# Kernel tuning notes

Measured on AMD Instinct MI355X. Metric: run time of the kernel, lower is better.

The kernel has to match this reference:

```python
import jax, jax.numpy as jnp
import numpy as np

LN_EPS = 1e-5
EPS = 1e-8
NUM_ITERS = 3

def _ln(x, w, b):
    mu = jnp.mean(x, axis=-1, keepdims=True)
    var = jnp.var(x, axis=-1, keepdims=True)
    return (x - mu) * jax.lax.rsqrt(var + LN_EPS) * w + b

def setup_inputs() -> dict:
    key = jax.random.key(0)
    ks = jax.random.split(key, 20)
    B, H, W, C = 16, 64, 64, 256
    D, S, HID, T = 128, 10, 256, 20
    g = lambda k, *shape: jax.random.normal(k, shape, dtype=jnp.float32) * 0.02
    return {
        'obs': jax.random.normal(ks[0], (B, H, W, C), dtype=jnp.float32),
        'noise': jax.random.normal(ks[1], (B, S, D), dtype=jnp.float32),
        'slots_mu': jax.random.normal(ks[2], (1, 1, D), dtype=jnp.float32),
        'slots_log_sigma': jax.random.normal(ks[3], (1, 1, D), dtype=jnp.float32) * 0.1,
        'ni_w': jnp.ones((C,), jnp.float32), 'ni_b': jnp.zeros((C,), jnp.float32),
        'ns_w': jnp.ones((D,), jnp.float32), 'ns_b': jnp.zeros((D,), jnp.float32),
        'nm_w': jnp.ones((D,), jnp.float32), 'nm_b': jnp.zeros((D,), jnp.float32),
        'Wq': g(ks[4], D, D), 'Wk': g(ks[5], C, D), 'Wv': g(ks[6], C, D),
        'mlp_w1': g(ks[7], D, 2 * D), 'mlp_b1': jnp.zeros((2 * D,), jnp.float32),
        'mlp_w2': g(ks[8], 2 * D, D), 'mlp_b2': jnp.zeros((D,), jnp.float32),
        'pd_w1': g(ks[9], D, HID), 'pd_b1': jnp.zeros((HID,), jnp.float32),
        'pd_w2': g(ks[10], HID, D), 'pd_b2': jnp.zeros((D,), jnp.float32),
        'tc_w': g(ks[11], D, T), 'tc_b': jnp.zeros((T,), jnp.float32),
    }

def reference(obs, noise, slots_mu, slots_log_sigma, ni_w, ni_b, ns_w, ns_b,
              nm_w, nm_b, Wq, Wk, Wv, mlp_w1, mlp_b1, mlp_w2, mlp_b2,
              pd_w1, pd_b1, pd_w2, pd_b2, tc_w, tc_b):
    B = obs.shape[0]
    x = obs.reshape(B, -1, obs.shape[-1])  # [B, N, C] (flatten H,W)
    D = Wq.shape[0]
    # slot init: mu + sigma * noise
    slots = slots_mu + jnp.exp(slots_log_sigma) * noise  # [B, S, D]
    x = _ln(x, ni_w, ni_b)
    k = x @ Wk  # [B, N, D]
    v = x @ Wv  # [B, N, D]
    scale = D ** -0.5
    attn = None
    for _ in range(NUM_ITERS):
        slots_prev = slots
        q = _ln(slots, ns_w, ns_b) @ Wq  # [B, S, D]
        logits = jnp.einsum('bsd,bnd->bsn', q, k) * scale
        attn = jax.nn.softmax(logits, axis=1)  # competitive over slots
        w = attn / (jnp.sum(attn, axis=-1, keepdims=True) + EPS)
        updates = jnp.einsum('bsn,bnd->bsd', w, v)
        slots = slots_prev + updates
        h = _ln(slots, nm_w, nm_b)
        slots = slots + (jax.nn.relu(h @ mlp_w1 + mlp_b1) @ mlp_w2 + mlp_b2)
    objects = jax.nn.relu(slots @ pd_w1 + pd_b1) @ pd_w2 + pd_b2
    object_types = slots @ tc_w + tc_b
    return objects, object_types
```

## Files before the change

kernel.cpp:

```cpp
#include <hip/hip_runtime.h>
#include <hip/hip_bf16.h>

typedef __hip_bfloat16 bf16;
typedef __attribute__((ext_vector_type(8))) short bf16x8;
typedef __attribute__((ext_vector_type(4))) float f32x4;

#define LN_EPS 1e-5f
#define ATT_EPS 1e-8f

__device__ __forceinline__ float bflo(unsigned u){ union{unsigned i;float f;}c; c.i=u<<16; return c.f; }
__device__ __forceinline__ float bfhi(unsigned u){ union{unsigned i;float f;}c; c.i=u&0xffff0000u; return c.f; }
__device__ __forceinline__ float bf2f(bf16 h){ return __bfloat162float(h); }
__device__ __forceinline__ unsigned f2bfbits(float f){
    bf16 h = __float2bfloat16(f);
    unsigned short s; __builtin_memcpy(&s, &h, 2);
    return (unsigned)s;
}

__device__ __forceinline__ float getv(const void* p, long i, int isf){
    if (isf) return ((const float*)p)[i];
    return bf2f(((const bf16*)p)[i]);
}
__device__ __forceinline__ void get8(const void* p, long i, int isf, float* o){
    if (isf){
        __builtin_memcpy(o, (const float*)p + i, 32);
    } else {
        unsigned u[4];
        __builtin_memcpy(u, (const bf16*)p + i, 16);
        o[0]=bflo(u[0]); o[1]=bfhi(u[0]); o[2]=bflo(u[1]); o[3]=bfhi(u[1]);
        o[4]=bflo(u[2]); o[5]=bfhi(u[2]); o[6]=bflo(u[3]); o[7]=bfhi(u[3]);
    }
}
__device__ __forceinline__ void load4f(const float* p, float* o){ __builtin_memcpy(o, p, 16); }
__device__ __forceinline__ void store4f(float* p, const float* v){ __builtin_memcpy(p, v, 16); }

__device__ __forceinline__ void wred2(float& a, float& b){
    #pragma unroll
    for (int m = 32; m > 0; m >>= 1){
        a += __shfl_xor(a, m, 64);
        b += __shfl_xor(b, m, 64);
    }
}

__global__ __launch_bounds__(256) void k_gmat(
        const void* __restrict__ Wq, const void* __restrict__ Wk,
        const void* __restrict__ niw, int* __restrict__ flag,
        float* __restrict__ G){
    unsigned u0; __builtin_memcpy(&u0, niw, 4);
    int isf = (u0 == 0x3F800000u) ? 1 : 0;
    if (blockIdx.x == 0 && threadIdx.x == 0) *flag = isf;
    int c = blockIdx.x, t = threadIdx.x;
    int d = t & 127, half = t >> 7;
    __shared__ float red2[2][128];
    float acc = 0.f;
    #pragma unroll
    for (int ch = 0; ch < 8; ch++){
        int dp = half*64 + ch*8;
        float wq8[8], wk8[8];
        get8(Wq, (long)d*128 + dp, isf, wq8);
        get8(Wk, (long)c*128 + dp, isf, wk8);
        #pragma unroll
        for (int j=0;j<8;j++) acc += wq8[j]*wk8[j];
    }
    red2[half][d] = acc;
    __syncthreads();
    if (t < 128)
        G[(long)t*256 + c] = (red2[0][t] + red2[1][t]) * 0.08838834764831845f;
}

__device__ __forceinline__ void phaseD(
        int b, int s, int t, const float* shlns, const float* __restrict__ G,
        const void* __restrict__ niw, const void* __restrict__ nib, int isf,
        bf16* __restrict__ wkqb, float* __restrict__ Ug, float* __restrict__ Vg,
        float* __restrict__ P2, float* __restrict__ t0g, float* __restrict__ t1g,
        float* redUV){
    int c = t;
    float kqc = 0.f;
    for (int d0 = 0; d0 < 128; d0 += 8){
        float l8[8];
        load4f(shlns + d0, l8); load4f(shlns + d0 + 4, l8 + 4);
        kqc += l8[0]*G[(long)(d0+0)*256+c] + l8[1]*G[(long)(d0+1)*256+c]
             + l8[2]*G[(long)(d0+2)*256+c] + l8[3]*G[(long)(d0+3)*256+c]
             + l8[4]*G[(long)(d0+4)*256+c] + l8[5]*G[(long)(d0+5)*256+c]
             + l8[6]*G[(long)(d0+6)*256+c] + l8[7]*G[(long)(d0+7)*256+c];
    }
    float wc = getv(niw, c, isf), bc = getv(nib, c, isf);
    float wkq = wc*kqc, vq = bc*kqc;
    float uu = wkq, vv = vq;
    wred2(uu, vv);
    int wid = t >> 6, lane = t & 63;
    if (lane == 0){ redUV[wid*2] = uu; redUV[wid*2+1] = vv; }
    wkqb[((long)b*16 + s)*256 + c] = __float2bfloat16(wkq);
    int bs = b*10 + s;
    P2[bs*256 + c] = 0.f;
    __syncthreads();
    if (t == 0){
        Ug[bs] = redUV[0] + redUV[2] + redUV[4] + redUV[6];
        Vg[bs] = redUV[1] + redUV[3] + redUV[5] + redUV[7];
        t0g[bs] = 0.f; t1g[bs] = 0.f;
    }
}

__global__ __launch_bounds__(256) void k_prep(
        const void* __restrict__ noise, const void* __restrict__ smu,
        const void* __restrict__ sls, const void* __restrict__ nsw,
        const void* __restrict__ nsb, const void* __restrict__ niw,
        const void* __restrict__ nib, const int* __restrict__ flag,
        const float* __restrict__ G, float* __restrict__ slots,
        bf16* __restrict__ wkqb, float* __restrict__ Ug, float* __restrict__ Vg,
        float* __restrict__ P2, float* __restrict__ t0g, float* __restrict__ t1g){
    int isf = *flag;
    int bs = blockIdx.x, t = threadIdx.x;
    int b = bs/10, s = bs - b*10;
    __shared__ __align__(16) float shlns[128];
    __shared__ float red[2][2];
    __shared__ float redUV[8];
    if (t < 128){
        float sv = getv(smu,t,isf) + __expf(getv(sls,t,isf)) * getv(noise,(long)bs*128+t,isf);
        slots[bs*128 + t] = sv;
        shlns[t] = sv;
        float su = sv, sq = sv*sv;
        wred2(su, sq);
        int wid = t >> 6, lane = t & 63;
        if (lane == 0){ red[wid][0]=su; red[wid][1]=sq; }
    }
    __syncthreads();
    if (t < 128){
        float su = red[0][0]+red[1][0], sq = red[0][1]+red[1][1];
        float m = su*(1.f/128.f), var = sq*(1.f/128.f) - m*m;
        float ri = rsqrtf(var + LN_EPS);
        shlns[t] = (shlns[t] - m)*ri*getv(nsw,t,isf) + getv(nsb,t,isf);
    }
    __syncthreads();
    phaseD(b, s, t, shlns, G, niw, nib, isf, wkqb, Ug, Vg, P2, t0g, t1g, redUV);
    if (s == 0){
        #pragma unroll
        for (int r = 10; r < 16; r++)
            wkqb[((long)b*16 + r)*256 + t] = __float2bfloat16(0.f);
    }
}

__global__ __launch_bounds__(256) void k_attn5(
        const void* __restrict__ obs, const bf16* __restrict__ wkqb,
        const float* __restrict__ Ug, const float* __restrict__ Vg,
        const int* __restrict__ flag, float* __restrict__ P2,
        float* __restrict__ t0g, float* __restrict__ t1g){
    int isf = *flag;
    int tile = blockIdx.x, b = blockIdx.y, t = threadIdx.x;
    int w = t >> 6, l = t & 63;
    __shared__ unsigned sxn[64*132];
    __shared__ __align__(16) float attnP[64*12];
    __shared__ float muri[128];
    __shared__ float denp0[4][16], denp1[4][16];

    if (isf){
        const float* gx = (const float*)obs + ((long)b*4096 + tile*64)*256;
        #pragma unroll
        for (int i = 0; i < 8; i++){
            int Ld = t*4 + i*1024;
            int px = Ld >> 7, col = Ld & 127;
            float f8[8];
            __builtin_memcpy(f8, gx + (long)px*256 + col*2, 32);
            unsigned pk[4];
            #pragma unroll
            for (int k2=0;k2<4;k2++)
                pk[k2] = (f2bfbits(f8[2*k2+1])<<16) | f2bfbits(f8[2*k2]);
            __builtin_memcpy(&sxn[px*132 + col], pk, 16);
        }
    } else {
        const unsigned* gx = (const unsigned*)obs + ((long)b*4096 + tile*64)*128;
        #pragma unroll
        for (int i = 0; i < 8; i++){
            int Ld = t*4 + i*1024;
            int px = Ld >> 7, col = Ld & 127;
            unsigned tmp[4];
            __builtin_memcpy(tmp, gx + Ld, 16);
            __builtin_memcpy(&sxn[px*132 + col], tmp, 16);
        }
    }
    bf16x8 bfr[8];
    {
        int s = l & 15, q = (l >> 4) & 3;
        const bf16* base = wkqb + ((long)b*16 + s)*256 + q*8;
        #pragma unroll
        for (int ks = 0; ks < 8; ks++)
            __builtin_memcpy(&bfr[ks], base + ks*32, 16);
    }
    __syncthreads();

    {
        int px = t >> 2, q = t & 3;
        float su = 0.f, sq = 0.f;
        #pragma unroll
        for (int j = 0; j < 8; j++){
            unsigned d4[4];
            __builtin_memcpy(d4, &sxn[px*132 + q*32 + j*4], 16);
            #pragma unroll
            for (int k2=0;k2<4;k2++){
                float a0 = bflo(d4[k2]), a1 = bfhi(d4[k2]);
                su += a0 + a1; sq += a0*a0 + a1*a1;
            }
        }
        su += __shfl_xor(su,1,64); sq += __shfl_xor(sq,1,64);
        su += __shfl_xor(su,2,64); sq += __shfl_xor(sq,2,64);
        if (q == 0){
            float m = su*(1.f/256.f);
            float ri = rsqrtf(sq*(1.f/256.f) - m*m + LN_EPS);
            muri[px*2] = m; muri[px*2+1] = ri;
        }
    }
    __syncthreads();

    f32x4 acc = {0.f,0.f,0.f,0.f};
    {
        int m = l & 15, q = (l >> 4) & 3;
        int rowbase = (w*16 + m)*132;
        #pragma unroll
        for (int ks = 0; ks < 8; ks++){
            bf16x8 af;
            __builtin_memcpy(&af, &sxn[rowbase + ks*16 + q*4], 16);
            acc = __builtin_amdgcn_mfma_f32_16x16x32_bf16(af, bfr[ks], acc, 0, 0, 0);
        }
    }

    {
        int col = l & 15, q = (l >> 4) & 3;
        float Uv = 0.f, Vv = 0.f;
        if (col < 10){ Uv = Ug[b*10 + col]; Vv = Vg[b*10 + col]; }
        float pden0 = 0.f, pden1 = 0.f;
        #pragma unroll
        for (int reg = 0; reg < 4; reg++){
            int px = w*16 + q*4 + reg;
            float mr[2]; __builtin_memcpy(mr, &muri[px*2], 8);
            float lg = (col < 10) ? (mr[1]*acc[reg] - mr[1]*mr[0]*Uv + Vv) : -1e30f;
            float mx = lg;
            mx = fmaxf(mx, __shfl_xor(mx,1,64));
            mx = fmaxf(mx, __shfl_xor(mx,2,64));
            mx = fmaxf(mx, __shfl_xor(mx,4,64));
            mx = fmaxf(mx, __shfl_xor(mx,8,64));
            float e = (col < 10) ? __expf(lg - mx) : 0.f;
            float sm = e;
            sm += __shfl_xor(sm,1,64);
            sm += __shfl_xor(sm,2,64);
            sm += __shfl_xor(sm,4,64);
            sm += __shfl_xor(sm,8,64);
            float a = e / sm;
            if (col < 10) attnP[px*12 + col] = a*mr[1];
            pden0 += a;
            pden1 += a*mr[1]*mr[0];
        }
        pden0 += __shfl_xor(pden0,16,64); pden0 += __shfl_xor(pden0,32,64);
        pden1 += __shfl_xor(pden1,16,64); pden1 += __shfl_xor(pden1,32,64);
        if (l < 10){ denp0[w][l] = pden0; denp1[w][l] = pden1; }
    }
    __syncthreads();
    if (t < 10){
        atomicAdd(&t0g[b*10 + t], denp0[0][t]+denp0[1][t]+denp0[2][t]+denp0[3][t]);
        atomicAdd(&t1g[b*10 + t], denp1[0][t]+denp1[1][t]+denp1[2][t]+denp1[3][t]);
    }

    {
        int c = t, ch = c >> 1, hh = c & 1;
        float pacc[10];
        #pragma unroll
        for (int s=0;s<10;s++) pacc[s]=0.f;
        for (int n = 0; n < 64; n++){
            unsigned d = sxn[n*132 + ch];
            float xv = hh ? bfhi(d) : bflo(d);
            float a[10];
            load4f(&attnP[n*12], a);
            load4f(&attnP[n*12 + 4], a + 4);
            __builtin_memcpy(a + 8, &attnP[n*12 + 8], 8);
            #pragma unroll
            for (int s=0;s<10;s++) pacc[s] += a[s]*xv;
        }
        #pragma unroll
        for (int s=0;s<10;s++) atomicAdd(&P2[b*2560 + s*256 + c], pacc[s]);
    }
}

__global__ __launch_bounds__(256) void k_slot(
        float* __restrict__ slots, float* __restrict__ P2,
        float* __restrict__ t0g, float* __restrict__ t1g,
        const void* __restrict__ Wv,
        const void* __restrict__ nmw, const void* __restrict__ nmb,
        const void* __restrict__ w1, const void* __restrict__ b1,
        const void* __restrict__ w2, const void* __restrict__ b2,
        const void* __restrict__ nsw, const void* __restrict__ nsb,
        const void* __restrict__ niw, const void* __restrict__ nib,
        const void* __restrict__ pw1, const void* __restrict__ pb1,
        const void* __restrict__ pw2, const void* __restrict__ pb2,
        const void* __restrict__ tw, const void* __restrict__ tb,
        const int* __restrict__ flag, const float* __restrict__ G,
        bf16* __restrict__ wkqb, float* __restrict__ Ug, float* __restrict__ Vg,
        void* __restrict__ out, int last){
    int isf = *flag;
    int bs = blockIdx.x, t = threadIdx.x;
    int b = bs/10, s = bs - b*10;
    __shared__ __align__(16) float pr[256];
    __shared__ __align__(16) float redA[16*128];
    __shared__ __align__(16) float redB[8*256];
    __shared__ __align__(16) float redT[8*32];
    __shared__ __align__(16) float hld[128];
    __shared__ __align__(16) float hid[256];
    __shared__ __align__(16) float shlns[128];
    __shared__ float red[4][2];
    __shared__ float redUV[8];

    float t0v = t0g[bs], t1v = t1g[bs];
    float wc = getv(niw,t,isf), bcv = getv(nib,t,isf);
    pr[t] = (P2[bs*256 + t] - t1v)*wc + t0v*bcv;
    __syncthreads();

    {
        int g = t & 15, ks = t >> 4;
        int d0 = g*8;
        float a8[8] = {0,0,0,0,0,0,0,0};
        #pragma unroll
        for (int j=0;j<16;j++){
            int c2 = ks*16 + j;
            float w8[8]; get8(Wv, (long)c2*128 + d0, isf, w8);
            float pv = pr[c2];
            #pragma unroll
            for (int k=0;k<8;k++) a8[k] += pv*w8[k];
        }
        store4f(&redA[ks*128 + d0], a8);
        store4f(&redA[ks*128 + d0 + 4], a8+4);
    }
    __syncthreads();
    float dv = t0v + ATT_EPS;
    float sn = 0.f;
    if (t < 128){
        float u = 0.f;
        #pragma unroll
        for (int ks=0;ks<16;ks++) u += redA[ks*128 + t];
        sn = slots[bs*128 + t] + u/dv;
    }
    float v = (t < 128) ? sn : 0.f;
    float su = v, sq = v*v;
    wred2(su, sq);
    int wid = t >> 6, lane = t & 63;
    if (lane == 0){ red[wid][0]=su; red[wid][1]=sq; }
    __syncthreads();
    su = red[0][0]+red[1][0]+red[2][0]+red[3][0];
    sq = red[0][1]+red[1][1]+red[2][1]+red[3][1];
    float mu = su*(1.f/128.f), var = sq*(1.f/128.f) - mu*mu;
    float rinv = rsqrtf(var + LN_EPS);
    if (t < 128) hld[t] = (v-mu)*rinv*getv(nmw,t,isf) + getv(nmb,t,isf);
    __syncthreads();

    {
        int g = t & 31, ks = t >> 5;
        int h0 = g*8;
        float a8[8] = {0,0,0,0,0,0,0,0};
        #pragma unroll
        for (int j=0;j<16;j++){
            int d = ks*16 + j;
            float w8[8]; get8(w1, (long)d*256 + h0, isf, w8);
            float hv = hld[d];
            #pragma unroll
            for (int k=0;k<8;k++) a8[k] += hv*w8[k];
        }
        store4f(&redB[ks*256 + h0], a8);
        store4f(&redB[ks*256 + h0 + 4], a8+4);
    }
    __syncthreads();
    {
        float hb = getv(b1,t,isf);
        #pragma unroll
        for (int ks=0;ks<8;ks++) hb += redB[ks*256 + t];
        hid[t] = fmaxf(hb, 0.f);
    }
    __syncthreads();

    {
        int g = t & 15, ks = t >> 4;
        int d0 = g*8;
        float a8[8] = {0,0,0,0,0,0,0,0};
        #pragma unroll
        for (int j=0;j<16;j++){
            int h = ks*16 + j;
            float w8[8]; get8(w2, (long)h*128 + d0, isf, w8);
            float hv = hid[h];
            #pragma unroll
            for (int k=0;k<8;k++) a8[k] += hv*w8[k];
        }
        store4f(&redA[ks*128 + d0], a8);
        store4f(&redA[ks*128 + d0 + 4], a8+4);
    }
    __syncthreads();
    float v2 = 0.f;
    if (t < 128){
        float o = getv(b2,t,isf);
        #pragma unroll
        for (int ks=0;ks<16;ks++) o += redA[ks*128 + t];
        v2 = sn + o;
    }

    if (!last){
        if (t < 128) slots[bs*128 + t] = v2;
        float s2 = v2, ss2 = v2*v2;
        wred2(s2, ss2);
        if (lane == 0){ red[wid][0]=s2; red[wid][1]=ss2; }
        __syncthreads();
        s2 = red[0][0]+red[1][0]+red[2][0]+red[3][0];
        ss2 = red[0][1]+red[1][1]+red[2][1]+red[3][1];
        float mu2 = s2*(1.f/128.f), var2 = ss2*(1.f/128.f) - mu2*mu2;
        float ri2 = rsqrtf(var2 + LN_EPS);
        if (t < 128)
            shlns[t] = (v2 - mu2)*ri2*getv(nsw,t,isf) + getv(nsb,t,isf);
        __syncthreads();
        phaseD(b, s, t, shlns, G, niw, nib, isf, wkqb, Ug, Vg, P2, t0g, t1g, redUV);
    } else {
        if (t < 128) shlns[t] = v2;
        __syncthreads();
        {
            int g = t & 31, ks = t >> 5;
            int h0 = g*8;
            float a8[8] = {0,0,0,0,0,0,0,0};
            #pragma unroll
            for (int j=0;j<16;j++){
                int d = ks*16 + j;
                float w8[8]; get8(pw1, (long)d*256 + h0, isf, w8);
                float hv = shlns[d];
                #pragma unroll
                for (int k=0;k<8;k++) a8[k] += hv*w8[k];
            }
            store4f(&redB[ks*256 + h0], a8);
            store4f(&redB[ks*256 + h0 + 4], a8+4);
        }
        __syncthreads();
        {
            float hb = getv(pb1,t,isf);
            #pragma unroll
            for (int ks=0;ks<8;ks++) hb += redB[ks*256 + t];
            hid[t] = fmaxf(hb, 0.f);
        }
        __syncthreads();
        {
            int g = t & 15, ks = t >> 4;
            int d0 = g*8;
            float a8[8] = {0,0,0,0,0,0,0,0};
            #pragma unroll
            for (int j=0;j<16;j++){
                int h = ks*16 + j;
                float w8[8]; get8(pw2, (long)h*128 + d0, isf, w8);
                float hv = hid[h];
                #pragma unroll
                for (int k=0;k<8;k++) a8[k] += hv*w8[k];
            }
            store4f(&redA[ks*128 + d0], a8);
            store4f(&redA[ks*128 + d0 + 4], a8+4);
        }
        {
            int ot = t & 31, ks = t >> 5;
            float a = 0.f;
            if (ot < 20){
                #pragma unroll
                for (int j=0;j<16;j++){
                    int d = ks*16 + j;
                    a += shlns[d]*getv(tw, (long)d*20 + ot, isf);
                }
            }
            redT[ks*32 + ot] = a;
        }
        __syncthreads();
        if (t < 128){
            float o = getv(pb2,t,isf);
            #pragma unroll
            for (int ks=0;ks<16;ks++) o += redA[ks*128 + t];
            int idx = bs*128 + t;
            if (isf) ((float*)out)[idx] = o; else ((bf16*)out)[idx] = __float2bfloat16(o);
        }
        if (t < 20){
            float o = getv(tb,t,isf);
            #pragma unroll
            for (int ks=0;ks<8;ks++) o += redT[ks*32 + t];
            int idx = 16*10*128 + bs*20 + t;
            if (isf) ((float*)out)[idx] = o; else ((bf16*)out)[idx] = __float2bfloat16(o);
        }
    }
}

extern "C" void kernel_launch(void* const* d_in, const int* in_sizes, int n_in,
                              void* d_out, int out_size, void* d_ws, size_t ws_size,
                              hipStream_t stream) {
    const void* obs   = d_in[0];
    const void* noise = d_in[1];
    const void* smu   = d_in[2];
    const void* sls   = d_in[3];
    const void* niw   = d_in[4];
    const void* nib   = d_in[5];
    const void* nsw   = d_in[6];
    const void* nsb   = d_in[7];
    const void* nmw   = d_in[8];
    const void* nmb   = d_in[9];
    const void* Wq    = d_in[10];
    const void* Wk    = d_in[11];
    const void* Wv    = d_in[12];
    const void* w1    = d_in[13];
    const void* b1    = d_in[14];
    const void* w2    = d_in[15];
    const void* b2    = d_in[16];
    const void* pw1   = d_in[17];
    const void* pb1   = d_in[18];
    const void* pw2   = d_in[19];
    const void* pb2   = d_in[20];
    const void* tw    = d_in[21];
    const void* tb    = d_in[22];

    char* ws = (char*)d_ws;
    int*   flag  = (int*)(ws);
    float* t0g   = (float*)(ws + 1024);
    float* t1g   = (float*)(ws + 2048);
    float* Ug    = (float*)(ws + 3072);
    float* Vg    = (float*)(ws + 4096);
    float* slots = (float*)(ws + 5120);
    float* P2    = (float*)(ws + 87040);
    float* G     = (float*)(ws + 250880);
    bf16*  wkqb  = (bf16*) (ws + 381952);

    k_gmat<<<256, 256, 0, stream>>>(Wq, Wk, niw, flag, G);
    k_prep<<<160, 256, 0, stream>>>(noise, smu, sls, nsw, nsb, niw, nib, flag, G,
                                    slots, wkqb, Ug, Vg, P2, t0g, t1g);
    for (int it = 0; it < 3; it++){
        k_attn5<<<dim3(64, 16), 256, 0, stream>>>(obs, wkqb, Ug, Vg, flag, P2, t0g, t1g);
        k_slot<<<160, 256, 0, stream>>>(slots, P2, t0g, t1g, Wv, nmw, nmb,
                                        w1, b1, w2, b2, nsw, nsb, niw, nib,
                                        pw1, pb1, pw2, pb2, tw, tb, flag, G,
                                        wkqb, Ug, Vg, d_out, (it == 2) ? 1 : 0);
    }
}
```

Before: 238.8 us.

## Precompute bf16 K/V projections once and stream compact KV in attention iterations

Adds a path that projects the layer-normed observations to bf16 K and V once, using a split hi/lo bf16 MFMA of the LN-folded weights. The three attention iterations then read this 256-wide bf16 KV buffer instead of re-reading the full obs tensor with the folded Wk·Wq form. Queries are computed per slot and stored as bf16, and per-tile partial updates are reduced in the slot kernel. The path is chosen only when the workspace is at least 41 MB, which costs an extra large buffer and some bf16 rounding of K, V and q.

```diff
diff --git a/kernel.cpp b/kernel.cpp
--- a/kernel.cpp
+++ b/kernel.cpp
@@ -41,6 +41,7 @@
         b += __shfl_xor(b, m, 64);
     }
 }
+
 
 __global__ __launch_bounds__(256) void k_gmat(
         const void* __restrict__ Wq, const void* __restrict__ Wk,
@@ -482,6 +483,454 @@
     }
 }
 
+
+__global__ __launch_bounds__(256) void k_wprep(
+        const void* __restrict__ Wk, const void* __restrict__ Wv,
+        const void* __restrict__ niw, const void* __restrict__ nib,
+        int* __restrict__ flag, bf16* __restrict__ Whit, bf16* __restrict__ Wlot,
+        float* __restrict__ Sg, float* __restrict__ Bg){
+    int d = blockIdx.x, t = threadIdx.x;
+    unsigned u0; __builtin_memcpy(&u0, niw, 4);
+    int isf = (u0 == 0x3F800000u) ? 1 : 0;
+    if (d == 0 && t == 0) *flag = isf;
+    float val = (d < 128) ? getv(Wk, (long)t*128 + d, isf)
+                          : getv(Wv, (long)t*128 + (d-128), isf);
+    float wp = getv(niw, t, isf) * val;
+    bf16 h = __float2bfloat16(wp);
+    Whit[(long)d*256 + t] = h;
+    Wlot[(long)d*256 + t] = __float2bfloat16(wp - bf2f(h));
+    float s = wp, bb = getv(nib, t, isf) * val;
+    wred2(s, bb);
+    __shared__ float r2[8];
+    int wv = t >> 6, ln = t & 63;
+    if (ln == 0){ r2[wv*2] = s; r2[wv*2+1] = bb; }
+    __syncthreads();
+    if (t == 0){ Sg[d] = r2[0]+r2[2]+r2[4]+r2[6]; Bg[d] = r2[1]+r2[3]+r2[5]+r2[7]; }
+}
+
+__global__ __launch_bounds__(256) void k_pre(
+        const void* __restrict__ obs, const int* __restrict__ flag,
+        const bf16* __restrict__ Whit, const bf16* __restrict__ Wlot,
+        const float* __restrict__ Sg, const float* __restrict__ Bg,
+        bf16* __restrict__ kvg){
+    int isf = *flag;
+    int tile = blockIdx.x, t = threadIdx.x;
+    __shared__ unsigned sxn[64*132];
+    __shared__ float muri[128];
+    __shared__ __align__(16) float sS[256];
+    __shared__ __align__(16) float sB[256];
+
+    if (isf){
+        const float* gx = (const float*)obs + (long)tile*64*256;
+        #pragma unroll
+        for (int i = 0; i < 8; i++){
+            int Ld = t*4 + i*1024;
+            int px = Ld >> 7, col = Ld & 127;
+            float f8[8];
+            __builtin_memcpy(f8, gx + (long)px*256 + col*2, 32);
+            unsigned pk[4];
+            #pragma unroll
+            for (int k2=0;k2<4;k2++)
+                pk[k2] = (f2bfbits(f8[2*k2+1])<<16) | f2bfbits(f8[2*k2]);
+            __builtin_memcpy(&sxn[px*132 + col], pk, 16);
+        }
+    } else {
+        const unsigned* gx = (const unsigned*)obs + (long)tile*64*128;
+        #pragma unroll
+        for (int i = 0; i < 8; i++){
+            int Ld = t*4 + i*1024;
+            int px = Ld >> 7, col = Ld & 127;
+            unsigned tmp[4];
+            __builtin_memcpy(tmp, gx + Ld, 16);
+            __builtin_memcpy(&sxn[px*132 + col], tmp, 16);
+        }
+    }
+    sS[t] = Sg[t]; sB[t] = Bg[t];
+    __syncthreads();
+    {
+        int px = t >> 2, q = t & 3;
+        float su = 0.f, sq = 0.f;
+        #pragma unroll
+        for (int j = 0; j < 8; j++){
+            unsigned d4[4];
+            __builtin_memcpy(d4, &sxn[px*132 + q*32 + j*4], 16);
+            #pragma unroll
+            for (int k2=0;k2<4;k2++){
+                float a0 = bflo(d4[k2]), a1 = bfhi(d4[k2]);
+                su += a0 + a1; sq += a0*a0 + a1*a1;
+            }
+        }
+        su += __shfl_xor(su,1,64); sq += __shfl_xor(sq,1,64);
+        su += __shfl_xor(su,2,64); sq += __shfl_xor(sq,2,64);
+        if (q == 0){
+            float m = su*(1.f/256.f);
+            float ri = rsqrtf(sq*(1.f/256.f) - m*m + LN_EPS);
+            muri[px*2] = m; muri[px*2+1] = ri;
+        }
+    }
+    __syncthreads();
+    {
+        int l = t & 63, w = t >> 6;
+        int mcol = l & 15, q4 = l >> 4;
+        unsigned* kvo = (unsigned*)kvg;
+        #pragma unroll
+        for (int mt = 0; mt < 4; mt++){
+            int dl = w*64 + mt*16 + mcol;
+            const bf16* ah = Whit + (long)dl*256 + q4*8;
+            const bf16* al = Wlot + (long)dl*256 + q4*8;
+            bf16x8 afh[8], afl[8];
+            #pragma unroll
+            for (int ks = 0; ks < 8; ks++){
+                __builtin_memcpy(&afh[ks], ah + ks*32, 16);
+                __builtin_memcpy(&afl[ks], al + ks*32, 16);
+            }
+            #pragma unroll
+            for (int ct = 0; ct < 4; ct++){
+                f32x4 a = {0.f,0.f,0.f,0.f};
+                int rb = (ct*16 + mcol)*132;
+                #pragma unroll
+                for (int ks = 0; ks < 8; ks++){
+                    bf16x8 bx;
+                    __builtin_memcpy(&bx, &sxn[rb + ks*16 + q4*4], 16);
+                    a = __builtin_amdgcn_mfma_f32_16x16x32_bf16(afh[ks], bx, a, 0,0,0);
+                    a = __builtin_amdgcn_mfma_f32_16x16x32_bf16(afl[ks], bx, a, 0,0,0);
+                }
+                int px = ct*16 + mcol;
+                int d0 = w*64 + mt*16 + q4*4;
+                float mu = muri[px*2], ri = muri[px*2+1];
+                float o0 = ri*a[0] - ri*mu*sS[d0+0] + sB[d0+0];
+                float o1 = ri*a[1] - ri*mu*sS[d0+1] + sB[d0+1];
+                float o2 = ri*a[2] - ri*mu*sS[d0+2] + sB[d0+2];
+                float o3 = ri*a[3] - ri*mu*sS[d0+3] + sB[d0+3];
+                long base = (long)tile*8192 + (long)px*128 + (d0>>1);
+                kvo[base]   = (f2bfbits(o1)<<16) | f2bfbits(o0);
+                kvo[base+1] = (f2bfbits(o3)<<16) | f2bfbits(o2);
+            }
+        }
+    }
+}
+
+__global__ __launch_bounds__(256) void k_prep2(
+        const void* __restrict__ noise, const void* __restrict__ smu,
+        const void* __restrict__ sls, const void* __restrict__ nsw,
+        const void* __restrict__ nsb, const void* __restrict__ Wq,
+        const int* __restrict__ flag, float* __restrict__ slots,
+        bf16* __restrict__ qb, float* __restrict__ t0g){
+    int isf = *flag;
+    int bs = blockIdx.x, t = threadIdx.x;
+    int b = bs/10, s = bs - b*10;
+    __shared__ __align__(16) float shlns[128];
+    __shared__ float red[2][2];
+    if (t < 128){
+        float sv = getv(smu,t,isf) + __expf(getv(sls,t,isf)) * getv(noise,(long)bs*128+t,isf);
+        slots[bs*128 + t] = sv;
+        shlns[t] = sv;
+        float su = sv, sq = sv*sv;
+        wred2(su, sq);
+        int wid = t >> 6, lane = t & 63;
+        if (lane == 0){ red[wid][0]=su; red[wid][1]=sq; }
+    }
+    __syncthreads();
+    if (t < 128){
+        float su = red[0][0]+red[1][0], sq = red[0][1]+red[1][1];
+        float m = su*(1.f/128.f), var = sq*(1.f/128.f) - m*m;
+        float ri = rsqrtf(var + LN_EPS);
+        shlns[t] = (shlns[t] - m)*ri*getv(nsw,t,isf) + getv(nsb,t,isf);
+    }
+    __syncthreads();
+    if (t < 128){
+        float acc = 0.f;
+        #pragma unroll 8
+        for (int dp = 0; dp < 128; dp++)
+            acc += shlns[dp] * getv(Wq, (long)dp*128 + t, isf);
+        qb[((long)b*16 + s)*128 + t] = __float2bfloat16(acc * 0.08838834764831845f);
+    }
+    if (t == 0) t0g[bs] = 0.f;
+    if (s == 0 && t < 128){
+        #pragma unroll
+        for (int r = 10; r < 16; r++)
+            qb[((long)b*16 + r)*128 + t] = __float2bfloat16(0.f);
+    }
+}
+
+__global__ __launch_bounds__(256) void k_attn6(
+        const bf16* __restrict__ kvg, const bf16* __restrict__ qb,
+        float* __restrict__ t0g, float* __restrict__ P2p){
+    int tile = blockIdx.x, b = blockIdx.y, t = threadIdx.x;
+    int w = t >> 6, l = t & 63;
+    __shared__ unsigned sxn[64*132];
+    __shared__ __align__(16) float attnP[64*16];
+    __shared__ float denp0[4][16];
+
+    const unsigned* gx = (const unsigned*)(kvg + ((long)b*4096 + tile*64)*256);
+    #pragma unroll
+    for (int i = 0; i < 8; i++){
+        int Ld = t*4 + i*1024;
+        int px = Ld >> 7, col = Ld & 127;
+        unsigned tmp[4];
+        __builtin_memcpy(tmp, gx + Ld, 16);
+        __builtin_memcpy(&sxn[px*132 + col], tmp, 16);
+    }
+    bf16x8 bfr[4];
+    {
+        int s = l & 15, q = (l >> 4) & 3;
+        const bf16* base = qb + ((long)b*16 + s)*128 + q*8;
+        #pragma unroll
+        for (int ks = 0; ks < 4; ks++)
+            __builtin_memcpy(&bfr[ks], base + ks*32, 16);
+    }
+    __syncthreads();
+
+    f32x4 acc = {0.f,0.f,0.f,0.f};
+    {
+        int m = l & 15, q = (l >> 4) & 3;
+        int rowbase = (w*16 + m)*132;
+        #pragma unroll
+        for (int ks = 0; ks < 4; ks++){
+            bf16x8 af;
+            __builtin_memcpy(&af, &sxn[rowbase + ks*16 + q*4], 16);
+            acc = __builtin_amdgcn_mfma_f32_16x16x32_bf16(af, bfr[ks], acc, 0, 0, 0);
+        }
+    }
+    {
+        int col = l & 15;
+        int q = (l >> 4) & 3;
+        float pden0 = 0.f;
+        #pragma unroll
+        for (int reg = 0; reg < 4; reg++){
+            int px = w*16 + q*4 + reg;
+            float lg = (col < 10) ? acc[reg] : -1e30f;
+            float mx = lg;
+            mx = fmaxf(mx, __shfl_xor(mx,1,64));
+            mx = fmaxf(mx, __shfl_xor(mx,2,64));
+            mx = fmaxf(mx, __shfl_xor(mx,4,64));
+            mx = fmaxf(mx, __shfl_xor(mx,8,64));
+            float e = (col < 10) ? __expf(lg - mx) : 0.f;
+            float sm = e;
+            sm += __shfl_xor(sm,1,64);
+            sm += __shfl_xor(sm,2,64);
+            sm += __shfl_xor(sm,4,64);
+            sm += __shfl_xor(sm,8,64);
+            float a = e / sm;
+            if (col < 10) attnP[px*16 + (col < 5 ? col : col + 3)] = a;
+            pden0 += a;
+        }
+        pden0 += __shfl_xor(pden0,16,64); pden0 += __shfl_xor(pden0,32,64);
+        if (l < 10) denp0[w][l] = pden0;
+    }
+    __syncthreads();
+    if (t < 10)
+        atomicAdd(&t0g[b*10 + t], denp0[0][t]+denp0[1][t]+denp0[2][t]+denp0[3][t]);
+
+    {
+        int d = t & 127, grp = t >> 7;
+        float p0=0.f,p1=0.f,p2=0.f,p3=0.f,p4=0.f;
+        int vdw = 64 + (d >> 1);
+        int hh = d & 1;
+        #pragma unroll 4
+        for (int n = 0; n < 64; n++){
+            unsigned dw = sxn[n*132 + vdw];
+            float xv = hh ? bfhi(dw) : bflo(dw);
+            float a4[4];
+            load4f(&attnP[n*16 + grp*8], a4);
+            float a5 = attnP[n*16 + grp*8 + 4];
+            p0 += a4[0]*xv; p1 += a4[1]*xv; p2 += a4[2]*xv; p3 += a4[3]*xv; p4 += a5*xv;
+        }
+        long base = ((long)(b*10 + grp*5)*64 + tile)*128 + d;
+        P2p[base]            = p0;
+        P2p[base +   64*128] = p1;
+        P2p[base + 2*64*128] = p2;
+        P2p[base + 3*64*128] = p3;
+        P2p[base + 4*64*128] = p4;
+    }
+}
+
+__global__ __launch_bounds__(256) void k_slot2(
+        float* __restrict__ slots, const float* __restrict__ P2p,
+        float* __restrict__ t0g,
+        const void* __restrict__ nmw, const void* __restrict__ nmb,
+        const void* __restrict__ w1, const void* __restrict__ b1,
+        const void* __restrict__ w2, const void* __restrict__ b2,
+        const void* __restrict__ nsw, const void* __restrict__ nsb,
+        const void* __restrict__ Wq,
+        const void* __restrict__ pw1, const void* __restrict__ pb1,
+        const void* __restrict__ pw2, const void* __restrict__ pb2,
+        const void* __restrict__ tw, const void* __restrict__ tb,
+        const int* __restrict__ flag, bf16* __restrict__ qb,
+        void* __restrict__ out, int last){
+    int isf = *flag;
+    int bs = blockIdx.x, t = threadIdx.x;
+    int b = bs/10, s = bs - b*10;
+    __shared__ __align__(16) float redA[16*128];
+    __shared__ __align__(16) float redB[8*256];
+    __shared__ __align__(16) float redT[8*32];
+    __shared__ __align__(16) float hld[128];
+    __shared__ __align__(16) float hid[256];
+    __shared__ __align__(16) float shlns[128];
+    __shared__ float red[4][2];
+
+    float t0v = t0g[bs];
+    float dv = t0v + ATT_EPS;
+    float sn = 0.f;
+    if (t < 128){
+        const float* pp = P2p + (long)bs*64*128 + t;
+        float u = 0.f;
+        #pragma unroll 8
+        for (int tl = 0; tl < 64; tl++) u += pp[tl*128];
+        sn = slots[bs*128 + t] + u/dv;
+    }
+    if (t == 0) t0g[bs] = 0.f;
+    float v = (t < 128) ? sn : 0.f;
+    float su = v, sq = v*v;
+    wred2(su, sq);
+    int wid = t >> 6, lane = t & 63;
+    if (lane == 0){ red[wid][0]=su; red[wid][1]=sq; }
+    __syncthreads();
+    su = red[0][0]+red[1][0]+red[2][0]+red[3][0];
+    sq = red[0][1]+red[1][1]+red[2][1]+red[3][1];
+    float mu = su*(1.f/128.f), var = sq*(1.f/128.f) - mu*mu;
+    float rinv = rsqrtf(var + LN_EPS);
+    if (t < 128) hld[t] = (v-mu)*rinv*getv(nmw,t,isf) + getv(nmb,t,isf);
+    __syncthreads();
+
+    {
+        int g = t & 31, ks = t >> 5;
+        int h0 = g*8;
+        float a8[8] = {0,0,0,0,0,0,0,0};
+        #pragma unroll
+        for (int j=0;j<16;j++){
+            int d = ks*16 + j;
+            float w8[8]; get8(w1, (long)d*256 + h0, isf, w8);
+            float hv = hld[d];
+            #pragma unroll
+            for (int k=0;k<8;k++) a8[k] += hv*w8[k];
+        }
+        store4f(&redB[ks*256 + h0], a8);
+        store4f(&redB[ks*256 + h0 + 4], a8+4);
+    }
+    __syncthreads();
+    {
+        float hb = getv(b1,t,isf);
+        #pragma unroll
+        for (int ks=0;ks<8;ks++) hb += redB[ks*256 + t];
+        hid[t] = fmaxf(hb, 0.f);
+    }
+    __syncthreads();
+    {
+        int g = t & 15, ks = t >> 4;
+        int d0 = g*8;
+        float a8[8] = {0,0,0,0,0,0,0,0};
+        #pragma unroll
+        for (int j=0;j<16;j++){
+            int h = ks*16 + j;
+            float w8[8]; get8(w2, (long)h*128 + d0, isf, w8);
+            float hv = hid[h];
+            #pragma unroll
+            for (int k=0;k<8;k++) a8[k] += hv*w8[k];
+        }
+        store4f(&redA[ks*128 + d0], a8);
+        store4f(&redA[ks*128 + d0 + 4], a8+4);
+    }
+    __syncthreads();
+    float v2 = 0.f;
+    if (t < 128){
+        float o = getv(b2,t,isf);
+        #pragma unroll
+        for (int ks=0;ks<16;ks++) o += redA[ks*128 + t];
+        v2 = sn + o;
+    }
+
+    if (!last){
+        if (t < 128) slots[bs*128 + t] = v2;
+        float s2 = v2, ss2 = v2*v2;
+        wred2(s2, ss2);
+        if (lane == 0){ red[wid][0]=s2; red[wid][1]=ss2; }
+        __syncthreads();
+        s2 = red[0][0]+red[1][0]+red[2][0]+red[3][0];
+        ss2 = red[0][1]+red[1][1]+red[2][1]+red[3][1];
+        float mu2 = s2*(1.f/128.f), var2 = ss2*(1.f/128.f) - mu2*mu2;
+        float ri2 = rsqrtf(var2 + LN_EPS);
+        if (t < 128)
+            shlns[t] = (v2 - mu2)*ri2*getv(nsw,t,isf) + getv(nsb,t,isf);
+        __syncthreads();
+        if (t < 128){
+            float acc2 = 0.f;
+            #pragma unroll 8
+            for (int dp = 0; dp < 128; dp++)
+                acc2 += shlns[dp] * getv(Wq, (long)dp*128 + t, isf);
+            qb[((long)b*16 + s)*128 + t] = __float2bfloat16(acc2 * 0.08838834764831845f);
+        }
+    } else {
+        if (t < 128) shlns[t] = v2;
+        __syncthreads();
+        {
+            int g = t & 31, ks = t >> 5;
+            int h0 = g*8;
+            float a8[8] = {0,0,0,0,0,0,0,0};
+            #pragma unroll
+            for (int j=0;j<16;j++){
+                int d = ks*16 + j;
+                float w8[8]; get8(pw1, (long)d*256 + h0, isf, w8);
+                float hv = shlns[d];
+                #pragma unroll
+                for (int k=0;k<8;k++) a8[k] += hv*w8[k];
+            }
+            store4f(&redB[ks*256 + h0], a8);
+            store4f(&redB[ks*256 + h0 + 4], a8+4);
+        }
+        __syncthreads();
+        {
+            float hb = getv(pb1,t,isf);
+            #pragma unroll
+            for (int ks=0;ks<8;ks++) hb += redB[ks*256 + t];
+            hid[t] = fmaxf(hb, 0.f);
+        }
+        __syncthreads();
+        {
+            int g = t & 15, ks = t >> 4;
+            int d0 = g*8;
+            float a8[8] = {0,0,0,0,0,0,0,0};
+            #pragma unroll
+            for (int j=0;j<16;j++){
+                int h = ks*16 + j;
+                float w8[8]; get8(pw2, (long)h*128 + d0, isf, w8);
+                float hv = hid[h];
+                #pragma unroll
+                for (int k=0;k<8;k++) a8[k] += hv*w8[k];
+            }
+            store4f(&redA[ks*128 + d0], a8);
+            store4f(&redA[ks*128 + d0 + 4], a8+4);
+        }
+        {
+            int ot = t & 31, ks = t >> 5;
+            float a = 0.f;
+            if (ot < 20){
+                #pragma unroll
+                for (int j=0;j<16;j++){
+                    int d = ks*16 + j;
+                    a += shlns[d]*getv(tw, (long)d*20 + ot, isf);
+                }
+            }
+            redT[ks*32 + ot] = a;
+        }
+        __syncthreads();
+        if (t < 128){
+            float o = getv(pb2,t,isf);
+            #pragma unroll
+            for (int ks=0;ks<16;ks++) o += redA[ks*128 + t];
+            int idx = bs*128 + t;
+            if (isf) ((float*)out)[idx] = o; else ((bf16*)out)[idx] = __float2bfloat16(o);
+        }
+        if (t < 20){
+            float o = getv(tb,t,isf);
+            #pragma unroll
+            for (int ks=0;ks<8;ks++) o += redT[ks*32 + t];
+            int idx = 16*10*128 + bs*20 + t;
+            if (isf) ((float*)out)[idx] = o; else ((bf16*)out)[idx] = __float2bfloat16(o);
+        }
+    }
+}
+
 extern "C" void kernel_launch(void* const* d_in, const int* in_sizes, int n_in,
                               void* d_out, int out_size, void* d_ws, size_t ws_size,
                               hipStream_t stream) {
@@ -510,24 +959,50 @@
     const void* tb    = d_in[22];
 
     char* ws = (char*)d_ws;
-    int*   flag  = (int*)(ws);
-    float* t0g   = (float*)(ws + 1024);
-    float* t1g   = (float*)(ws + 2048);
-    float* Ug    = (float*)(ws + 3072);
-    float* Vg    = (float*)(ws + 4096);
-    float* slots = (float*)(ws + 5120);
-    float* P2    = (float*)(ws + 87040);
-    float* G     = (float*)(ws + 250880);
-    bf16*  wkqb  = (bf16*) (ws + 381952);
-
-    k_gmat<<<256, 256, 0, stream>>>(Wq, Wk, niw, flag, G);
-    k_prep<<<160, 256, 0, stream>>>(noise, smu, sls, nsw, nsb, niw, nib, flag, G,
-                                    slots, wkqb, Ug, Vg, P2, t0g, t1g);
-    for (int it = 0; it < 3; it++){
-        k_attn5<<<dim3(64, 16), 256, 0, stream>>>(obs, wkqb, Ug, Vg, flag, P2, t0g, t1g);
-        k_slot<<<160, 256, 0, stream>>>(slots, P2, t0g, t1g, Wv, nmw, nmb,
-                                        w1, b1, w2, b2, nsw, nsb, niw, nib,
-                                        pw1, pb1, pw2, pb2, tw, tb, flag, G,
-                                        wkqb, Ug, Vg, d_out, (it == 2) ? 1 : 0);
-    }
-}
+
+    if (ws_size >= (size_t)(41u << 20)) {
+        int*   flag  = (int*)(ws);
+        float* t0g   = (float*)(ws + 1024);
+        float* Sg    = (float*)(ws + 2048);
+        float* Bg    = (float*)(ws + 3072);
+        float* slots = (float*)(ws + 4096);
+        bf16*  qb    = (bf16*) (ws + 86016);
+        bf16*  Whit  = (bf16*) (ws + 151552);
+        bf16*  Wlot  = (bf16*) (ws + 282624);
+        float* P2p   = (float*)(ws + 413696);
+        bf16*  kvg   = (bf16*) (ws + 5656576);
+
+        k_wprep<<<256, 256, 0, stream>>>(Wk, Wv, niw, nib, flag, Whit, Wlot, Sg, Bg);
+        k_pre<<<1024, 256, 0, stream>>>(obs, flag, Whit, Wlot, Sg, Bg, kvg);
+        k_prep2<<<160, 256, 0, stream>>>(noise, smu, sls, nsw, nsb, Wq, flag,
+                                         slots, qb, t0g);
+        for (int it = 0; it < 3; it++){
+            k_attn6<<<dim3(64, 16), 256, 0, stream>>>(kvg, qb, t0g, P2p);
+            k_slot2<<<160, 256, 0, stream>>>(slots, P2p, t0g, nmw, nmb,
+                                             w1, b1, w2, b2, nsw, nsb, Wq,
+                                             pw1, pb1, pw2, pb2, tw, tb, flag,
+                                             qb, d_out, (it == 2) ? 1 : 0);
+        }
+    } else {
+        int*   flag  = (int*)(ws);
+        float* t0g   = (float*)(ws + 1024);
+        float* t1g   = (float*)(ws + 2048);
+        float* Ug    = (float*)(ws + 3072);
+        float* Vg    = (float*)(ws + 4096);
+        float* slots = (float*)(ws + 5120);
+        float* P2    = (float*)(ws + 87040);
+        float* G     = (float*)(ws + 250880);
+        bf16*  wkqb  = (bf16*) (ws + 381952);
+
+        k_gmat<<<256, 256, 0, stream>>>(Wq, Wk, niw, flag, G);
+        k_prep<<<160, 256, 0, stream>>>(noise, smu, sls, nsw, nsb, niw, nib, flag, G,
+                                        slots, wkqb, Ug, Vg, P2, t0g, t1g);
+        for (int it = 0; it < 3; it++){
+            k_attn5<<<dim3(64, 16), 256, 0, stream>>>(obs, wkqb, Ug, Vg, flag, P2, t0g, t1g);
+            k_slot<<<160, 256, 0, stream>>>(slots, P2, t0g, t1g, Wv, nmw, nmb,
+                                            w1, b1, w2, b2, nsw, nsb, niw, nib,
+                                            pw1, pb1, pw2, pb2, tw, tb, flag, G,
+                                            wkqb, Ug, Vg, d_out, (it == 2) ? 1 : 0);
+        }
+    }
+}
```

New measurement: 279.8 us. 1.17x slower.
